# Performance work log

Hardware: AMD Instinct MI355X
Metric: run time of the kernel (lower is better)

## Reference

```python
import jax, jax.numpy as jnp
import numpy as np

OUT_H, OUT_W = 7, 7
SR = 2            # sampling_ratio
SCALE = 0.25      # spatial_scale


def setup_inputs() -> dict:
    key = jax.random.key(0)
    k1, k2, k3, k4, k5 = jax.random.split(key, 5)
    inp = jax.random.normal(k1, (2, 256, 200, 200), dtype=jnp.float32)
    K = 512
    cx = jax.random.uniform(k2, (K,), minval=100.0, maxval=700.0)
    cy = jax.random.uniform(k3, (K,), minval=100.0, maxval=700.0)
    wh = jax.random.uniform(k4, (K, 2), minval=32.0, maxval=192.0)
    x1 = jnp.clip(cx - wh[:, 0] / 2, 0.0, 798.0)
    x2 = jnp.clip(cx + wh[:, 0] / 2, x1 + 1.0, 800.0)
    y1 = jnp.clip(cy - wh[:, 1] / 2, 0.0, 798.0)
    y2 = jnp.clip(cy + wh[:, 1] / 2, y1 + 1.0, 800.0)
    bi = jax.random.randint(k5, (K,), 0, 2).astype(jnp.float32)
    rois = jnp.stack([bi, x1, y1, x2, y2], axis=1).astype(jnp.float32)
    return {"input": inp, "rois": rois}


def _sample_coords(start, bin_size, pooled, sr):
    # bin-major sample ordering: [bin0_s0, bin0_s1, bin1_s0, ...] as in the torch code
    p = jnp.arange(pooled, dtype=jnp.float32)
    i = jnp.arange(sr, dtype=jnp.float32)
    grid = bin_size[:, None, None] * p[None, :, None] \
         + (bin_size / sr)[:, None, None] * (i + 0.5)[None, None, :]
    K = start.shape[0]
    return start[:, None] + grid.reshape(K, pooled * sr)  # [K, pooled*sr]


def _roi_align(input, rois):
    H, W = input.shape[2], input.shape[3]
    K, C = rois.shape[0], input.shape[1]
    b = rois[:, 0].astype(jnp.int32)
    x1, y1, x2, y2 = (rois[:, j] * SCALE for j in (1, 2, 3, 4))
    roi_w = jnp.maximum(x2 - x1, 1.0)
    roi_h = jnp.maximum(y2 - y1, 1.0)
    y = _sample_coords(y1, roi_h / OUT_H, OUT_H, SR)  # [K, OUT_H*SR]
    x = _sample_coords(x1, roi_w / OUT_W, OUT_W, SR)  # [K, OUT_W*SR]
    # original zeroes an entire ROI if any sample falls outside [-1, H] x [-1, W]
    valid = jnp.all((y >= -1.0) & (y <= H), axis=1) & \
            jnp.all((x >= -1.0) & (x <= W), axis=1)   # [K]
    yc = jnp.clip(y, 0.0, H - 1.0)
    xc = jnp.clip(x, 0.0, W - 1.0)
    yl = jnp.floor(yc)
    xl = jnp.floor(xc)
    yh = jnp.clip(yl + 1.0, 0.0, H - 1.0)
    xh = jnp.clip(xl + 1.0, 0.0, W - 1.0)
    ly = yc - yl
    lx = xc - xl
    hy = 1.0 - ly
    hx = 1.0 - lx
    yl_i, yh_i = yl.astype(jnp.int32), yh.astype(jnp.int32)
    xl_i, xh_i = xl.astype(jnp.int32), xh.astype(jnp.int32)
    bi = b[:, None, None]  # [K,1,1]

    def gather(yi, xi):
        # mixed advanced indexing -> [K, Sy, Sx, C]
        return input[bi, :, yi[:, :, None], xi[:, None, :]]

    v1 = gather(yl_i, xl_i)
    v2 = gather(yl_i, xh_i)
    v3 = gather(yh_i, xl_i)
    v4 = gather(yh_i, xh_i)
    w1 = hy[:, :, None] * hx[:, None, :]
    w2 = hy[:, :, None] * lx[:, None, :]
    w3 = ly[:, :, None] * hx[:, None, :]
    w4 = ly[:, :, None] * lx[:, None, :]
    res = (w1[..., None] * v1 + w2[..., None] * v2 +
           w3[..., None] * v3 + w4[..., None] * v4)  # [K, Sy, Sx, C]
    # average SRxSR samples per bin; original hardcodes division by 4 (== SR*SR here)
    res = res.reshape(K, OUT_H, SR, OUT_W, SR, C).sum(axis=(2, 4)) / 4.0
    res = res * valid[:, None, None, None].astype(res.dtype)
    return jnp.transpose(res, (0, 3, 1, 2))  # [K, C, OUT_H, OUT_W]


def reference(input, rois):
    return _roi_align(input, rois)
```

## Files before the change

### kernel.cpp

```cpp
#include <hip/hip_runtime.h>

#define IN_H 200
#define IN_W 200
#define NCH  256
#define NROI 512
#define OUT_HW 49
#define PLANE (IN_H * IN_W)

__global__ __launch_bounds__(256) void transpose_bf16_kernel(
    const float* __restrict__ in, ushort* __restrict__ nhwc) {
  __shared__ ushort t[64][260];
  const int blk = blockIdx.x;
  const int hwt = blk % 625;
  const int b   = blk / 625;
  const int w = threadIdx.x >> 6, l = threadIdx.x & 63;
  const int hw0 = hwt * 64;

  const float* src = in + (size_t)b * NCH * PLANE + hw0;
#pragma unroll 4
  for (int i = 0; i < 64; ++i) {
    const int c = w * 64 + i;
    const float v = src[(size_t)c * PLANE + l];
    const unsigned u = __float_as_uint(v);
    const unsigned r = (u + 0x7fffu + ((u >> 16) & 1u)) >> 16;
    t[l][c] = (ushort)r;
  }
  __syncthreads();

  ushort* dst = nhwc + ((size_t)b * PLANE + hw0) * NCH;
#pragma unroll
  for (int m = threadIdx.x; m < 64 * 64; m += 256) {
    const int h = m >> 6;
    const int q = m & 63;
    *(ushort4*)(dst + (size_t)h * NCH + q * 4) = *(const ushort4*)&t[h][q * 4];
  }
}

__global__ __launch_bounds__(512) void roi_nhwc_bf16_kernel(
    const ushort* __restrict__ nhwc,
    const float* __restrict__ rois,
    float* __restrict__ out) {
  __shared__ float sout[NCH * OUT_HW];

  const int k  = blockIdx.x;
  const int t  = threadIdx.x;
  const int pg = t >> 6;
  const int c0 = (t & 63) * 4;

  const float* r = rois + k * 5;
  const int   b   = (int)r[0];
  const float x1s = r[1] * 0.25f;
  const float y1s = r[2] * 0.25f;
  const float x2s = r[3] * 0.25f;
  const float y2s = r[4] * 0.25f;
  const float roi_w = fmaxf(x2s - x1s, 1.0f);
  const float roi_h = fmaxf(y2s - y1s, 1.0f);
  const float bw = roi_w / 7.0f;
  const float bh = roi_h / 7.0f;

  const bool valid = (y1s + 0.25f * bh >= -1.0f) && (y1s + 6.75f * bh <= (float)IN_H) &&
                     (x1s + 0.25f * bw >= -1.0f) && (x1s + 6.75f * bw <= (float)IN_W);
  const float scale = valid ? 0.25f : 0.0f;

  const ushort* base = nhwc + (size_t)b * PLANE * NCH;

  for (int p = pg; p < OUT_HW; p += 8) {
    const int ph = p / 7;
    const int pw = p - ph * 7;
    const float ybase = y1s + bh * (float)ph;
    const float xbase = x1s + bw * (float)pw;

    float acc0 = 0.0f, acc1 = 0.0f, acc2 = 0.0f, acc3 = 0.0f;
#pragma unroll
    for (int iy = 0; iy < 2; ++iy) {
      const float y  = ybase + (bh * 0.5f) * ((float)iy + 0.5f);
      const float yc = fminf(fmaxf(y, 0.0f), (float)(IN_H - 1));
      const float ylf = floorf(yc);
      const int   yl  = (int)ylf;
      const int   yh  = min(yl + 1, IN_H - 1);
      const float ly  = yc - ylf;
      const float hy  = 1.0f - ly;
      const ushort* rowl = base + (size_t)yl * IN_W * NCH + c0;
      const ushort* rowh = base + (size_t)yh * IN_W * NCH + c0;
#pragma unroll
      for (int ix = 0; ix < 2; ++ix) {
        const float x  = xbase + (bw * 0.5f) * ((float)ix + 0.5f);
        const float xc = fminf(fmaxf(x, 0.0f), (float)(IN_W - 1));
        const float xlf = floorf(xc);
        const int   xl  = (int)xlf;
        const int   xh  = min(xl + 1, IN_W - 1);
        const float lx  = xc - xlf;
        const float hx  = 1.0f - lx;

        const ushort4 u1 = *(const ushort4*)(rowl + (size_t)xl * NCH);
        const ushort4 u2 = *(const ushort4*)(rowl + (size_t)xh * NCH);
        const ushort4 u3 = *(const ushort4*)(rowh + (size_t)xl * NCH);
        const ushort4 u4 = *(const ushort4*)(rowh + (size_t)xh * NCH);

        const float w1 = hy * hx, w2 = hy * lx, w3 = ly * hx, w4 = ly * lx;
#define BF(us) __uint_as_float(((unsigned)(us)) << 16)
        acc0 += w1 * BF(u1.x) + w2 * BF(u2.x) + w3 * BF(u3.x) + w4 * BF(u4.x);
        acc1 += w1 * BF(u1.y) + w2 * BF(u2.y) + w3 * BF(u3.y) + w4 * BF(u4.y);
        acc2 += w1 * BF(u1.z) + w2 * BF(u2.z) + w3 * BF(u3.z) + w4 * BF(u4.z);
        acc3 += w1 * BF(u1.w) + w2 * BF(u2.w) + w3 * BF(u3.w) + w4 * BF(u4.w);
#undef BF
      }
    }
    sout[(c0 + 0) * OUT_HW + p] = acc0 * scale;
    sout[(c0 + 1) * OUT_HW + p] = acc1 * scale;
    sout[(c0 + 2) * OUT_HW + p] = acc2 * scale;
    sout[(c0 + 3) * OUT_HW + p] = acc3 * scale;
  }
  __syncthreads();

  float4* o4 = (float4*)(out + (size_t)k * NCH * OUT_HW);
  const float4* s4 = (const float4*)sout;
  for (int m = t; m < (NCH * OUT_HW) / 4; m += 512) o4[m] = s4[m];
}

__global__ __launch_bounds__(256) void roi_align_fallback(
    const float* __restrict__ input,
    const float* __restrict__ rois,
    float* __restrict__ out) {
  const int blk  = blockIdx.x;
  const int k    = blk >> 6;
  const int cg   = blk & 63;
  const int wave = threadIdx.x >> 6;
  const int lane = threadIdx.x & 63;
  const int c    = (cg << 2) + wave;

  const float* r = rois + k * 5;
  const int   b   = (int)r[0];
  const float x1s = r[1] * 0.25f;
  const float y1s = r[2] * 0.25f;
  const float roi_w = fmaxf(r[3] * 0.25f - x1s, 1.0f);
  const float roi_h = fmaxf(r[4] * 0.25f - y1s, 1.0f);
  const float bw = roi_w / 7.0f;
  const float bh = roi_h / 7.0f;
  const bool valid = (y1s + 0.25f * bh >= -1.0f) && (y1s + 6.75f * bh <= (float)IN_H) &&
                     (x1s + 0.25f * bw >= -1.0f) && (x1s + 6.75f * bw <= (float)IN_W);
  if (lane >= OUT_HW) return;
  const int ph = lane / 7;
  const int pw = lane - ph * 7;
  const float* plane = input + ((size_t)(b * NCH + c)) * PLANE;
  const float ybase = y1s + bh * (float)ph;
  const float xbase = x1s + bw * (float)pw;
  float acc = 0.0f;
#pragma unroll
  for (int iy = 0; iy < 2; ++iy) {
    const float y  = ybase + (bh * 0.5f) * ((float)iy + 0.5f);
    const float yc = fminf(fmaxf(y, 0.0f), (float)(IN_H - 1));
    const float ylf = floorf(yc);
    const int yl = (int)ylf;
    const int yh = min(yl + 1, IN_H - 1);
    const float ly = yc - ylf, hy = 1.0f - ly;
#pragma unroll
    for (int ix = 0; ix < 2; ++ix) {
      const float x  = xbase + (bw * 0.5f) * ((float)ix + 0.5f);
      const float xc = fminf(fmaxf(x, 0.0f), (float)(IN_W - 1));
      const float xlf = floorf(xc);
      const int xl = (int)xlf;
      const int xh = min(xl + 1, IN_W - 1);
      const float lx = xc - xlf, hx = 1.0f - lx;
      const float* row_l = plane + yl * IN_W;
      const float* row_h = plane + yh * IN_W;
      acc += hy * hx * row_l[xl] + hy * lx * row_l[xh] +
             ly * hx * row_h[xl] + ly * lx * row_h[xh];
    }
  }
  out[((size_t)k * NCH + c) * OUT_HW + lane] = valid ? acc * 0.25f : 0.0f;
}

extern "C" void kernel_launch(void* const* d_in, const int* in_sizes, int n_in,
                              void* d_out, int out_size, void* d_ws, size_t ws_size,
                              hipStream_t stream) {
  const float* input = (const float*)d_in[0];
  const float* rois  = (const float*)d_in[1];
  float* out = (float*)d_out;

  const size_t need = (size_t)2 * PLANE * NCH * sizeof(ushort);
  if (ws_size >= need) {
    ushort* nhwc = (ushort*)d_ws;
    transpose_bf16_kernel<<<2 * 625, 256, 0, stream>>>(input, nhwc);
    roi_nhwc_bf16_kernel<<<NROI, 512, 0, stream>>>(nhwc, rois, out);
  } else {
    roi_align_fallback<<<NROI * (NCH / 4), 256, 0, stream>>>(input, rois, out);
  }
}
```

Measured before the change: 47.40 us.

## Sort ROIs by batch and spatial bucket to improve L2 locality across XCDs

Adds a single-block kernel that buckets ROIs by batch index and an 8x8 grid of center positions, then writes a permutation. The ROI kernel maps block IDs so that blocks landing on the same XCD (blockIdx mod 8) process spatially adjacent ROIs, which should raise L2 reuse of the shared NHWC feature rows. This costs an extra serial kernel launch with an O(n) rank loop per thread, and changes the order of output writes.

```diff
diff --git a/kernel.cpp b/kernel.cpp
--- a/kernel.cpp
+++ b/kernel.cpp
@@ -36,13 +36,46 @@
   }
 }
 
+__global__ __launch_bounds__(512) void roi_sort_kernel(
+    const float* __restrict__ rois, int* __restrict__ perm) {
+  __shared__ int keys[NROI];
+  __shared__ int offs[128];
+  __shared__ int hist[128];
+  const int t = threadIdx.x;
+  {
+    const float* r = rois + t * 5;
+    const int b = (int)r[0];
+    const float cx = (r[1] + r[3]) * 0.125f;
+    const float cy = (r[2] + r[4]) * 0.125f;
+    int xb = (int)(cx * 0.04f);
+    int yb = (int)(cy * 0.04f);
+    xb = min(max(xb, 0), 7);
+    yb = min(max(yb, 0), 7);
+    keys[t] = (b << 6) | (yb << 3) | xb;
+  }
+  if (t < 128) hist[t] = 0;
+  __syncthreads();
+  atomicAdd(&hist[keys[t]], 1);
+  __syncthreads();
+  if (t == 0) {
+    int s = 0;
+    for (int i = 0; i < 128; ++i) { offs[i] = s; s += hist[i]; }
+  }
+  __syncthreads();
+  const int myk = keys[t];
+  int rank = 0;
+  for (int j = 0; j < t; ++j) rank += (keys[j] == myk) ? 1 : 0;
+  perm[offs[myk] + rank] = t;
+}
+
 __global__ __launch_bounds__(512) void roi_nhwc_bf16_kernel(
     const ushort* __restrict__ nhwc,
     const float* __restrict__ rois,
+    const int* __restrict__ perm,
     float* __restrict__ out) {
   __shared__ float sout[NCH * OUT_HW];
 
-  const int k  = blockIdx.x;
+  const int k  = perm[(blockIdx.x & 7) * 64 + (blockIdx.x >> 3)];
   const int t  = threadIdx.x;
   const int pg = t >> 6;
   const int c0 = (t & 63) * 4;
@@ -178,11 +211,14 @@
   const float* rois  = (const float*)d_in[1];
   float* out = (float*)d_out;
 
-  const size_t need = (size_t)2 * PLANE * NCH * sizeof(ushort);
+  const size_t nhwc_bytes = (size_t)2 * PLANE * NCH * sizeof(ushort);
+  const size_t need = nhwc_bytes + NROI * sizeof(int);
   if (ws_size >= need) {
     ushort* nhwc = (ushort*)d_ws;
+    int* perm = (int*)((char*)d_ws + nhwc_bytes);
     transpose_bf16_kernel<<<2 * 625, 256, 0, stream>>>(input, nhwc);
-    roi_nhwc_bf16_kernel<<<NROI, 512, 0, stream>>>(nhwc, rois, out);
+    roi_sort_kernel<<<1, 512, 0, stream>>>(rois, perm);
+    roi_nhwc_bf16_kernel<<<NROI, 512, 0, stream>>>(nhwc, rois, perm, out);
   } else {
     roi_align_fallback<<<NROI * (NCH / 4), 256, 0, stream>>>(input, rois, out);
   }
```

Measured after the change: 49.61 us. 1.05x slower.
